# Performance work log

Hardware: AMD Instinct MI355X
Metric: run time of the kernel (lower is better)

Reference implementation:

```python
import jax, jax.numpy as jnp
import numpy as np

DIM = 768
HEADS = 12
HEAD_DIM = DIM // HEADS          # 64
DIM_HALF = HEAD_DIM // 2         # 32
SPATIAL = 3


def _rope_cos_sin(grid, voxel_size, theta):
    """grid: static tuple of ints (len SPATIAL); voxel_size: [SPATIAL] float;
    theta: [H, DIM_HALF] per-head frequency spectrum.
    Returns cos, sin of shape [H, N, DIM_HALF] where N = prod(grid)."""
    axes = [jnp.arange(g, dtype=theta.dtype) for g in grid]
    mesh = jnp.meshgrid(*axes, indexing='ij')
    coords = jnp.stack([m.reshape(-1) for m in mesh], axis=-1) * voxel_size  # [N, S] physical coords
    axis_idx = np.arange(DIM_HALF) % len(grid)        # round-robin freq->axis assignment
    pos = coords[:, axis_idx]                          # [N, DIM_HALF]
    ang = pos[None, :, :] * theta[:, None, :]          # [H, N, DIM_HALF]
    return jnp.cos(ang), jnp.sin(ang)


def _rope_apply(t, cos, sin):
    # t: [B, H, N, D]; cos/sin: [H, N, DIM_HALF] broadcast over batch
    t1, t2 = jnp.split(t, 2, axis=-1)
    return jnp.concatenate([t1 * cos - t2 * sin, t1 * sin + t2 * cos], axis=-1)


def setup_inputs() -> dict:
    key = jax.random.key(0)
    k_x, k_qkv, k_proj, k_b = jax.random.split(key, 4)
    B, N = 2, 8 * 16 * 16
    x = jax.random.normal(k_x, (B, N, DIM), dtype=jnp.float32)
    voxel_size = jnp.ones((SPATIAL,), dtype=jnp.float32)
    # nn.Linear weights are [out_features, in_features]
    w_qkv = jax.random.normal(k_qkv, (3 * DIM, DIM), dtype=jnp.float32) * (DIM ** -0.5)
    w_proj = jax.random.normal(k_proj, (DIM, DIM), dtype=jnp.float32) * (DIM ** -0.5)
    b_proj = jax.random.normal(k_b, (DIM,), dtype=jnp.float32) * 0.02
    # learnable per-head base frequencies: theta_j = 10000^{-j/dim_half}
    base = (1.0 / (10000.0 ** (np.arange(DIM_HALF, dtype=np.float32) / DIM_HALF)))
    theta = jnp.asarray(np.tile(base[None, :], (HEADS, 1)))  # [H, DIM_HALF]
    return {"x": x, "voxel_size": voxel_size, "w_qkv": w_qkv, "w_proj": w_proj,
            "b_proj": b_proj, "theta": theta, "grid_d": 8, "grid_h": 16, "grid_w": 16}


def reference(x, voxel_size, w_qkv, w_proj, b_proj, theta, grid_d, grid_h, grid_w):
    B, N, dim = x.shape
    H, D = HEADS, HEAD_DIM
    qkv = jnp.einsum('bnd,ed->bne', x, w_qkv).reshape(B, N, 3, H, D)
    qkv = jnp.transpose(qkv, (2, 0, 3, 1, 4))           # [3, B, H, N, D]
    q, k, v = qkv[0], qkv[1], qkv[2]
    cos, sin = _rope_cos_sin((grid_d, grid_h, grid_w), voxel_size, theta)
    q = _rope_apply(q, cos, sin)
    k = _rope_apply(k, cos, sin)
    scale = 1.0 / np.sqrt(D).astype(np.float32)
    attn = jax.nn.softmax(jnp.einsum('bhnd,bhmd->bhnm', q, k) * scale, axis=-1)
    out = jnp.einsum('bhnm,bhmd->bhnd', attn, v)        # [B, H, N, D]
    out = jnp.transpose(out, (0, 2, 1, 3)).reshape(B, N, dim)
    return out @ w_proj.T + b_proj
```

## Files before the change

kernel.cpp:

```cpp
#include <hip/hip_runtime.h>
#include <stdint.h>

#define DIM 768
#define NHEADS 12
#define HDIM 64
#define DHALF 32
#define NTOK 2048
#define QKVN 2304
#define LOG2E 1.44269504088896340736f

typedef unsigned short u16;
typedef unsigned int u32;
typedef __bf16 bf16x8 __attribute__((ext_vector_type(8)));
typedef short s16x8 __attribute__((ext_vector_type(8)));
typedef float f32x4 __attribute__((ext_vector_type(4)));

__device__ __forceinline__ f32x4 f4zero() { f32x4 z = {0.f, 0.f, 0.f, 0.f}; return z; }

__device__ __forceinline__ u16 f2bf(float f) {
    u32 u = __builtin_bit_cast(u32, f);
    u32 r = (u + 0x7FFFu + ((u >> 16) & 1u)) >> 16;
    return (u16)r;
}

__device__ __forceinline__ void gld_lds16(void* lds, const void* g) {
    __builtin_amdgcn_global_load_lds((const __attribute__((address_space(1))) u32*)g,
                                     (__attribute__((address_space(3))) u32*)lds,
                                     16, 0, 0);
}

__global__ __launch_bounds__(256) void cast3_f32_to_bf16(const float* __restrict__ a, u16* __restrict__ oa, int na4,
                                                         const float* __restrict__ b, u16* __restrict__ ob, int nb4,
                                                         const float* __restrict__ c, u16* __restrict__ oc, int nc4) {
    int i = blockIdx.x * 256 + threadIdx.x;
    const float* src;
    u16* dst;
    int j = i;
    if (i < na4) { src = a; dst = oa; }
    else if (i < na4 + nb4) { src = b; dst = ob; j = i - na4; }
    else if (i < na4 + nb4 + nc4) { src = c; dst = oc; j = i - na4 - nb4; }
    else return;
    float4 v = ((const float4*)src)[j];
    u32 w0 = (u32)f2bf(v.x) | ((u32)f2bf(v.y) << 16);
    u32 w1 = (u32)f2bf(v.z) | ((u32)f2bf(v.w) << 16);
    ((uint2*)dst)[j] = make_uint2(w0, w1);
}

__global__ __launch_bounds__(256) void gemm_bt(const u16* __restrict__ A, const u16* __restrict__ Bm,
                                               float* __restrict__ C, const float* __restrict__ bias,
                                               int M, int N, int K) {
    __shared__ __align__(16) u16 sA[2][128 * 32];
    __shared__ __align__(16) u16 sB[2][128 * 32];
    const int t = threadIdx.x;
    const int wave = t >> 6, lane = t & 63;
    const int quad = lane >> 4, l16 = lane & 15;
    const int bm = blockIdx.y * 128, bn = blockIdx.x * 128;
    const int wr = wave >> 1, wc = wave & 1;

    f32x4 acc[4][4];
#pragma unroll
    for (int i = 0; i < 4; i++)
#pragma unroll
        for (int j = 0; j < 4; j++) acc[i][j] = f4zero();

    auto stage = [&](int k0, int bi) {
#pragma unroll
        for (int r = 0; r < 2; ++r) {
            int c = (r * 4 + wave) * 64 + lane;
            int row = c >> 2, kc = c & 3;
            gld_lds16((char*)&sA[bi][0] + (size_t)(r * 4 + wave) * 1024,
                      A + (size_t)(bm + row) * K + k0 + kc * 8);
            gld_lds16((char*)&sB[bi][0] + (size_t)(r * 4 + wave) * 1024,
                      Bm + (size_t)(bn + row) * K + k0 + kc * 8);
        }
    };

    stage(0, 0);
    int cur = 0;
    for (int k0 = 0; k0 < K; k0 += 32) {
        __syncthreads();
        if (k0 + 32 < K) stage(k0 + 32, cur ^ 1);
        const u16* pA = &sA[cur][0];
        const u16* pB = &sB[cur][0];
        bf16x8 af[4], bfr[4];
#pragma unroll
        for (int mb = 0; mb < 4; mb++)
            af[mb] = *(const bf16x8*)(pA + (wr * 64 + mb * 16 + l16) * 32 + quad * 8);
#pragma unroll
        for (int nb = 0; nb < 4; nb++)
            bfr[nb] = *(const bf16x8*)(pB + (wc * 64 + nb * 16 + l16) * 32 + quad * 8);
#pragma unroll
        for (int mb = 0; mb < 4; mb++)
#pragma unroll
            for (int nb = 0; nb < 4; nb++)
                acc[mb][nb] = __builtin_amdgcn_mfma_f32_16x16x32_bf16(af[mb], bfr[nb], acc[mb][nb], 0, 0, 0);
        cur ^= 1;
    }
#pragma unroll
    for (int mb = 0; mb < 4; mb++)
#pragma unroll
        for (int nb = 0; nb < 4; nb++) {
            int col = bn + wc * 64 + nb * 16 + l16;
            float bv = bias ? bias[col] : 0.f;
#pragma unroll
            for (int r = 0; r < 4; r++) {
                int row = bm + wr * 64 + mb * 16 + quad * 4 + r;
                C[(size_t)row * N + col] = acc[mb][nb][r] + bv;
            }
        }
}

__global__ __launch_bounds__(256) void gemm_qkv_rope(const u16* __restrict__ A, const u16* __restrict__ Bm,
                                                     const float* __restrict__ voxel,
                                                     const float* __restrict__ theta,
                                                     const int* __restrict__ gh_p, const int* __restrict__ gw_p,
                                                     u16* __restrict__ q_s, u16* __restrict__ k_s,
                                                     u16* __restrict__ vT, int M) {
    __shared__ __align__(16) u16 sA[2][128 * 32];
    __shared__ __align__(16) u16 sB[2][128 * 32];
    const int t = threadIdx.x;
    const int wave = t >> 6, lane = t & 63;
    const int quad = lane >> 4, l16 = lane & 15;
    const int bm = blockIdx.y * 128, bn = blockIdx.x * 128;
    const int wr = wave >> 1, wc = wave & 1;
    const int K = DIM;

    f32x4 acc[4][4];
#pragma unroll
    for (int i = 0; i < 4; i++)
#pragma unroll
        for (int j = 0; j < 4; j++) acc[i][j] = f4zero();

    auto stage = [&](int k0, int bi) {
#pragma unroll
        for (int r = 0; r < 2; ++r) {
            int c = (r * 4 + wave) * 64 + lane;
            int row = c >> 2, kc = c & 3;
            gld_lds16((char*)&sA[bi][0] + (size_t)(r * 4 + wave) * 1024,
                      A + (size_t)(bm + row) * K + k0 + kc * 8);
            gld_lds16((char*)&sB[bi][0] + (size_t)(r * 4 + wave) * 1024,
                      Bm + (size_t)(bn + row) * K + k0 + kc * 8);
        }
    };

    stage(0, 0);
    int cur = 0;
    for (int k0 = 0; k0 < K; k0 += 32) {
        __syncthreads();
        if (k0 + 32 < K) stage(k0 + 32, cur ^ 1);
        const u16* pA = &sA[cur][0];
        const u16* pB = &sB[cur][0];
        bf16x8 af[4], bfr[4];
#pragma unroll
        for (int mb = 0; mb < 4; mb++)
            af[mb] = *(const bf16x8*)(pA + (wr * 64 + mb * 16 + l16) * 32 + quad * 8);
#pragma unroll
        for (int nb = 0; nb < 4; nb++)
            bfr[nb] = *(const bf16x8*)(pB + (wc * 64 + nb * 16 + l16) * 32 + quad * 8);
#pragma unroll
        for (int mb = 0; mb < 4; mb++)
#pragma unroll
            for (int nb = 0; nb < 4; nb++)
                acc[mb][nb] = __builtin_amdgcn_mfma_f32_16x16x32_bf16(af[mb], bfr[nb], acc[mb][nb], 0, 0, 0);
        cur ^= 1;
    }

    const int col0 = bn + wc * 64;
    const int typ = col0 / DIM;
    const int h = (col0 % DIM) >> 6;
    const int b = bm / NTOK;
    const int n0 = (bm % NTOK) + wr * 64;
    const size_t bh = (size_t)b * NHEADS + h;

    if (typ == 2) {
        int nt = n0 >> 6;
        u16* base = vT + (bh * 64 + (size_t)nt * 2) * 2048;
#pragma unroll
        for (int c2 = 0; c2 < 2; c2++)
#pragma unroll
            for (int nb = 0; nb < 4; nb++) {
                u32 w0 = (u32)f2bf(acc[2 * c2][nb][0]) | ((u32)f2bf(acc[2 * c2][nb][1]) << 16);
                u32 w1 = (u32)f2bf(acc[2 * c2][nb][2]) | ((u32)f2bf(acc[2 * c2][nb][3]) << 16);
                u32 w2 = (u32)f2bf(acc[2 * c2 + 1][nb][0]) | ((u32)f2bf(acc[2 * c2 + 1][nb][1]) << 16);
                u32 w3 = (u32)f2bf(acc[2 * c2 + 1][nb][2]) | ((u32)f2bf(acc[2 * c2 + 1][nb][3]) << 16);
                *(uint4*)(base + (size_t)c2 * 2048 + nb * 512 + lane * 8) = make_uint4(w0, w1, w2, w3);
            }
    } else {
        const int gh = *gh_p, gw = *gw_p;
        const float qsc = (typ == 0) ? 0.125f * LOG2E : 1.0f;
        const float th0 = theta[h * DHALF + l16];
        const float th1 = theta[h * DHALF + 16 + l16];
        const int ax0 = l16 % 3, ax1 = (16 + l16) % 3;
        const float vx0 = voxel[ax0], vx1 = voxel[ax1];
#pragma unroll
        for (int mb = 0; mb < 4; mb++)
#pragma unroll
            for (int r = 0; r < 4; r++) {
                int n = n0 + mb * 16 + quad * 4 + r;
                int xw = n % gw;
                int rem = n / gw;
                int yh = rem % gh;
                int zd = rem / gh;
                float c0 = (float)(ax0 == 0 ? zd : (ax0 == 1 ? yh : xw)) * vx0;
                float c1 = (float)(ax1 == 0 ? zd : (ax1 == 1 ? yh : xw)) * vx1;
                float s0, co0, s1, co1;
                __sincosf(c0 * th0, &s0, &co0);
                __sincosf(c1 * th1, &s1, &co1);
                float t1a = acc[mb][0][r], t2a = acc[mb][2][r];
                float o1a = (t1a * co0 - t2a * s0) * qsc, o2a = (t1a * s0 + t2a * co0) * qsc;
                float t1b = acc[mb][1][r], t2b = acc[mb][3][r];
                float o1b = (t1b * co1 - t2b * s1) * qsc, o2b = (t1b * s1 + t2b * co1) * qsc;
                if (typ == 0) {
                    u16* dq = q_s + (bh * NTOK + n) * HDIM;
                    dq[l16] = f2bf(o1a);
                    dq[l16 + DHALF] = f2bf(o2a);
                    dq[16 + l16] = f2bf(o1b);
                    dq[48 + l16] = f2bf(o2b);
                } else {
                    int tile_i = n >> 6;
                    int k16 = quad * 4 + r;
                    size_t baseo = bh * (size_t)NTOK * HDIM + (size_t)tile_i * 4096 + mb * 1024;
                    int j = l16 & 7;
                    size_t oa = baseo + (size_t)(((l16 >> 3) * 16 + k16) * 8 + j);
                    size_t ob = baseo + (size_t)((((2 + (l16 >> 3)) * 16) + k16) * 8 + j);
                    k_s[oa] = f2bf(o1a);
                    k_s[oa + 512] = f2bf(o2a);
                    k_s[ob] = f2bf(o1b);
                    k_s[ob + 512] = f2bf(o2b);
                }
            }
    }
}

__global__ __launch_bounds__(256) void flash_attn(const u16* __restrict__ Q, const u16* __restrict__ Kp,
                                                  const u16* __restrict__ Vp, u16* __restrict__ Out, int NBH) {
    int i = blockIdx.x;
    int bh_i = i % NBH;
    int qt = i / NBH;
    int b = bh_i / NHEADS, h = bh_i % NHEADS;
    int t = threadIdx.x, wave = t >> 6, lane = t & 63, quad = lane >> 4, l16 = lane & 15;
    size_t bh = (size_t)b * NHEADS + h;
    const u16* Qb = Q + bh * NTOK * HDIM;
    const u16* Kb = Kp + bh * NTOK * HDIM;
    const u16* Vb = Vp + bh * NTOK * HDIM;

    __shared__ __align__(16) u16 smem[2][8192];

    const int q0 = qt * 64 + wave * 16;
    bf16x8 qf[2];
#pragma unroll
    for (int kc = 0; kc < 2; kc++)
        qf[kc] = *(const bf16x8*)(Qb + (size_t)(q0 + l16) * HDIM + kc * 32 + quad * 8);

    s16x8 ov;
#pragma unroll
    for (int j = 0; j < 8; j++) ov[j] = (l16 == 0) ? (short)0x3F80 : (short)0;

    f32x4 o[5];
#pragma unroll
    for (int db = 0; db < 5; db++) o[db] = f4zero();

    auto stage = [&](int kt, int bi) {
        const u16* Kg = Kb + (size_t)kt * 4096;
        const u16* Vg = Vb + (size_t)kt * 4096;
        u16* buf = &smem[bi][0];
#pragma unroll
        for (int s = 0; s < 2; s++) {
            gld_lds16(buf + (wave * 2 + s) * 512, Kg + (wave * 2 + s) * 512 + lane * 8);
            gld_lds16(buf + 4096 + (wave * 2 + s) * 512, Vg + (wave * 2 + s) * 512 + lane * 8);
        }
    };

    stage(0, 0);
    int cur = 0;
    for (int kt = 0; kt < NTOK / 64; ++kt) {
        __syncthreads();
        if (kt + 1 < NTOK / 64) stage(kt + 1, cur ^ 1);
        const u16* sK = &smem[cur][0];
        const u16* sV = &smem[cur][4096];
#pragma unroll
        for (int c = 0; c < 2; ++c) {
            bf16x8 kf[2][2];
#pragma unroll
            for (int kb2 = 0; kb2 < 2; kb2++)
#pragma unroll
                for (int kc = 0; kc < 2; kc++)
                    kf[kb2][kc] = *(const bf16x8*)(sK + ((c * 2 + kb2) * 2 + kc) * 512 + lane * 8);
            s16x8 bv[4];
#pragma unroll
            for (int db = 0; db < 4; db++)
                bv[db] = *(const s16x8*)(sV + c * 2048 + db * 512 + lane * 8);
            f32x4 st0, st1;
            {
                f32x4 z = f4zero();
                z = __builtin_amdgcn_mfma_f32_16x16x32_bf16(kf[0][0], qf[0], z, 0, 0, 0);
                st0 = __builtin_amdgcn_mfma_f32_16x16x32_bf16(kf[0][1], qf[1], z, 0, 0, 0);
                f32x4 z2 = f4zero();
                z2 = __builtin_amdgcn_mfma_f32_16x16x32_bf16(kf[1][0], qf[0], z2, 0, 0, 0);
                st1 = __builtin_amdgcn_mfma_f32_16x16x32_bf16(kf[1][1], qf[1], z2, 0, 0, 0);
            }
            bf16x8 pb;
#pragma unroll
            for (int r = 0; r < 4; r++) {
                pb[r] = (__bf16)__builtin_exp2f(st0[r]);
                pb[r + 4] = (__bf16)__builtin_exp2f(st1[r]);
            }
#pragma unroll
            for (int db = 0; db < 4; db++)
                o[db] = __builtin_amdgcn_mfma_f32_16x16x32_bf16(pb, __builtin_bit_cast(bf16x8, bv[db]),
                                                                o[db], 0, 0, 0);
            o[4] = __builtin_amdgcn_mfma_f32_16x16x32_bf16(pb, __builtin_bit_cast(bf16x8, ov),
                                                           o[4], 0, 0, 0);
        }
        cur ^= 1;
    }

#pragma unroll
    for (int r = 0; r < 4; r++) {
        float s = __shfl(o[4][r], lane & 48);
        float inv = 1.0f / s;
        int n = q0 + quad * 4 + r;
        u16* dst = Out + ((size_t)b * NTOK + n) * DIM + h * HDIM + l16;
#pragma unroll
        for (int db = 0; db < 4; db++)
            dst[db * 16] = f2bf(o[db][r] * inv);
    }
}

extern "C" void kernel_launch(void* const* d_in, const int* in_sizes, int n_in,
                              void* d_out, int out_size, void* d_ws, size_t ws_size,
                              hipStream_t stream) {
    const float* x = (const float*)d_in[0];
    const float* voxel = (const float*)d_in[1];
    const float* w_qkv = (const float*)d_in[2];
    const float* w_proj = (const float*)d_in[3];
    const float* b_proj = (const float*)d_in[4];
    const float* theta = (const float*)d_in[5];
    const int* gh_p = (const int*)d_in[7];
    const int* gw_p = (const int*)d_in[8];
    const int B = in_sizes[0] / (NTOK * DIM);
    const int M = B * NTOK;

    char* p = (char*)d_ws;
    u16* xb = (u16*)p;       p += (size_t)M * DIM * 2;
    u16* wqkvb = (u16*)p;    p += (size_t)3 * DIM * DIM * 2;
    u16* wprojb = (u16*)p;   p += (size_t)DIM * DIM * 2;
    u16* q_s = (u16*)p;      p += (size_t)M * DIM * 2;
    u16* k_s = (u16*)p;      p += (size_t)M * DIM * 2;
    u16* vT = (u16*)p;       p += (size_t)M * DIM * 2;
    u16* attn = (u16*)p;     p += (size_t)M * DIM * 2;

    int na4 = M * DIM / 4, nb4 = 3 * DIM * DIM / 4, nc4 = DIM * DIM / 4;
    cast3_f32_to_bf16<<<dim3((na4 + nb4 + nc4 + 255) / 256), 256, 0, stream>>>(
        x, xb, na4, w_qkv, wqkvb, nb4, w_proj, wprojb, nc4);

    gemm_qkv_rope<<<dim3(QKVN / 128, M / 128), 256, 0, stream>>>(
        xb, wqkvb, voxel, theta, gh_p, gw_p, q_s, k_s, vT, M);

    flash_attn<<<dim3((B * NHEADS * NTOK) / 64), 256, 0, stream>>>(q_s, k_s, vT, attn, B * NHEADS);

    gemm_bt<<<dim3(DIM / 128, M / 128), 256, 0, stream>>>(attn, wprojb, (float*)d_out, b_proj, M, DIM, DIM);
}
```

Measured before the change: 180.4 us.

## Shrink GEMM tiles to raise block count for QKV and projection GEMMs

The output-projection GEMM moves from 128x128 tiles to 64x64 tiles, and the QKV+RoPE GEMM moves to 128x64 tiles with each wave owning 32 rows of a single head. The epilogue index math for the V-transpose and K-swizzle layouts is reworked to match the new wave ownership. The aim is to launch more blocks so the many compute units are better filled (the projection previously had only 192 blocks). The cost is less operand reuse per block and more global and LDS traffic per FLOP.

Measured after the change: 176.6 us. 1.02x faster.

```diff
diff --git a/kernel.cpp b/kernel.cpp
--- a/kernel.cpp
+++ b/kernel.cpp
@@ -49,30 +49,25 @@
 __global__ __launch_bounds__(256) void gemm_bt(const u16* __restrict__ A, const u16* __restrict__ Bm,
                                                float* __restrict__ C, const float* __restrict__ bias,
                                                int M, int N, int K) {
-    __shared__ __align__(16) u16 sA[2][128 * 32];
-    __shared__ __align__(16) u16 sB[2][128 * 32];
+    __shared__ __align__(16) u16 sA[2][64 * 32];
+    __shared__ __align__(16) u16 sB[2][64 * 32];
     const int t = threadIdx.x;
     const int wave = t >> 6, lane = t & 63;
     const int quad = lane >> 4, l16 = lane & 15;
-    const int bm = blockIdx.y * 128, bn = blockIdx.x * 128;
+    const int bm = blockIdx.y * 64, bn = blockIdx.x * 64;
     const int wr = wave >> 1, wc = wave & 1;
 
-    f32x4 acc[4][4];
-#pragma unroll
-    for (int i = 0; i < 4; i++)
-#pragma unroll
-        for (int j = 0; j < 4; j++) acc[i][j] = f4zero();
+    f32x4 acc[2][2];
+#pragma unroll
+    for (int i = 0; i < 2; i++)
+#pragma unroll
+        for (int j = 0; j < 2; j++) acc[i][j] = f4zero();
 
     auto stage = [&](int k0, int bi) {
-#pragma unroll
-        for (int r = 0; r < 2; ++r) {
-            int c = (r * 4 + wave) * 64 + lane;
-            int row = c >> 2, kc = c & 3;
-            gld_lds16((char*)&sA[bi][0] + (size_t)(r * 4 + wave) * 1024,
-                      A + (size_t)(bm + row) * K + k0 + kc * 8);
-            gld_lds16((char*)&sB[bi][0] + (size_t)(r * 4 + wave) * 1024,
-                      Bm + (size_t)(bn + row) * K + k0 + kc * 8);
-        }
+        gld_lds16((char*)&sA[bi][0] + wave * 1024,
+                  A + (size_t)(bm + wave * 16 + (lane >> 2)) * K + k0 + (lane & 3) * 8);
+        gld_lds16((char*)&sB[bi][0] + wave * 1024,
+                  Bm + (size_t)(bn + wave * 16 + (lane >> 2)) * K + k0 + (lane & 3) * 8);
     };
 
     stage(0, 0);
@@ -82,29 +77,29 @@
         if (k0 + 32 < K) stage(k0 + 32, cur ^ 1);
         const u16* pA = &sA[cur][0];
         const u16* pB = &sB[cur][0];
-        bf16x8 af[4], bfr[4];
-#pragma unroll
-        for (int mb = 0; mb < 4; mb++)
-            af[mb] = *(const bf16x8*)(pA + (wr * 64 + mb * 16 + l16) * 32 + quad * 8);
-#pragma unroll
-        for (int nb = 0; nb < 4; nb++)
-            bfr[nb] = *(const bf16x8*)(pB + (wc * 64 + nb * 16 + l16) * 32 + quad * 8);
-#pragma unroll
-        for (int mb = 0; mb < 4; mb++)
-#pragma unroll
-            for (int nb = 0; nb < 4; nb++)
+        bf16x8 af[2], bfr[2];
+#pragma unroll
+        for (int mb = 0; mb < 2; mb++)
+            af[mb] = *(const bf16x8*)(pA + (wr * 32 + mb * 16 + l16) * 32 + quad * 8);
+#pragma unroll
+        for (int nb = 0; nb < 2; nb++)
+            bfr[nb] = *(const bf16x8*)(pB + (wc * 32 + nb * 16 + l16) * 32 + quad * 8);
+#pragma unroll
+        for (int mb = 0; mb < 2; mb++)
+#pragma unroll
+            for (int nb = 0; nb < 2; nb++)
                 acc[mb][nb] = __builtin_amdgcn_mfma_f32_16x16x32_bf16(af[mb], bfr[nb], acc[mb][nb], 0, 0, 0);
         cur ^= 1;
     }
 #pragma unroll
-    for (int mb = 0; mb < 4; mb++)
-#pragma unroll
-        for (int nb = 0; nb < 4; nb++) {
-            int col = bn + wc * 64 + nb * 16 + l16;
+    for (int mb = 0; mb < 2; mb++)
+#pragma unroll
+        for (int nb = 0; nb < 2; nb++) {
+            int col = bn + wc * 32 + nb * 16 + l16;
             float bv = bias ? bias[col] : 0.f;
 #pragma unroll
             for (int r = 0; r < 4; r++) {
-                int row = bm + wr * 64 + mb * 16 + quad * 4 + r;
+                int row = bm + wr * 32 + mb * 16 + quad * 4 + r;
                 C[(size_t)row * N + col] = acc[mb][nb][r] + bv;
             }
         }
@@ -117,30 +112,28 @@
                                                      u16* __restrict__ q_s, u16* __restrict__ k_s,
                                                      u16* __restrict__ vT, int M) {
     __shared__ __align__(16) u16 sA[2][128 * 32];
-    __shared__ __align__(16) u16 sB[2][128 * 32];
+    __shared__ __align__(16) u16 sB[2][64 * 32];
     const int t = threadIdx.x;
     const int wave = t >> 6, lane = t & 63;
     const int quad = lane >> 4, l16 = lane & 15;
-    const int bm = blockIdx.y * 128, bn = blockIdx.x * 128;
-    const int wr = wave >> 1, wc = wave & 1;
+    const int bm = blockIdx.y * 128, bn = blockIdx.x * 64;
     const int K = DIM;
 
-    f32x4 acc[4][4];
-#pragma unroll
-    for (int i = 0; i < 4; i++)
+    f32x4 acc[2][4];
+#pragma unroll
+    for (int i = 0; i < 2; i++)
 #pragma unroll
         for (int j = 0; j < 4; j++) acc[i][j] = f4zero();
 
     auto stage = [&](int k0, int bi) {
 #pragma unroll
-        for (int r = 0; r < 2; ++r) {
-            int c = (r * 4 + wave) * 64 + lane;
-            int row = c >> 2, kc = c & 3;
-            gld_lds16((char*)&sA[bi][0] + (size_t)(r * 4 + wave) * 1024,
-                      A + (size_t)(bm + row) * K + k0 + kc * 8);
-            gld_lds16((char*)&sB[bi][0] + (size_t)(r * 4 + wave) * 1024,
-                      Bm + (size_t)(bn + row) * K + k0 + kc * 8);
-        }
+        for (int s = 0; s < 2; ++s) {
+            int ci = wave * 2 + s;
+            gld_lds16((char*)&sA[bi][0] + ci * 1024,
+                      A + (size_t)(bm + ci * 16 + (lane >> 2)) * K + k0 + (lane & 3) * 8);
+        }
+        gld_lds16((char*)&sB[bi][0] + wave * 1024,
+                  Bm + (size_t)(bn + wave * 16 + (lane >> 2)) * K + k0 + (lane & 3) * 8);
     };
 
     stage(0, 0);
@@ -150,41 +143,39 @@
         if (k0 + 32 < K) stage(k0 + 32, cur ^ 1);
         const u16* pA = &sA[cur][0];
         const u16* pB = &sB[cur][0];
-        bf16x8 af[4], bfr[4];
-#pragma unroll
-        for (int mb = 0; mb < 4; mb++)
-            af[mb] = *(const bf16x8*)(pA + (wr * 64 + mb * 16 + l16) * 32 + quad * 8);
+        bf16x8 af[2], bfr[4];
+#pragma unroll
+        for (int mb = 0; mb < 2; mb++)
+            af[mb] = *(const bf16x8*)(pA + (wave * 32 + mb * 16 + l16) * 32 + quad * 8);
 #pragma unroll
         for (int nb = 0; nb < 4; nb++)
-            bfr[nb] = *(const bf16x8*)(pB + (wc * 64 + nb * 16 + l16) * 32 + quad * 8);
-#pragma unroll
-        for (int mb = 0; mb < 4; mb++)
+            bfr[nb] = *(const bf16x8*)(pB + (nb * 16 + l16) * 32 + quad * 8);
+#pragma unroll
+        for (int mb = 0; mb < 2; mb++)
 #pragma unroll
             for (int nb = 0; nb < 4; nb++)
                 acc[mb][nb] = __builtin_amdgcn_mfma_f32_16x16x32_bf16(af[mb], bfr[nb], acc[mb][nb], 0, 0, 0);
         cur ^= 1;
     }
 
-    const int col0 = bn + wc * 64;
+    const int col0 = bn;
     const int typ = col0 / DIM;
     const int h = (col0 % DIM) >> 6;
     const int b = bm / NTOK;
-    const int n0 = (bm % NTOK) + wr * 64;
+    const int n0 = (bm % NTOK) + wave * 32;
     const size_t bh = (size_t)b * NHEADS + h;
 
     if (typ == 2) {
-        int nt = n0 >> 6;
-        u16* base = vT + (bh * 64 + (size_t)nt * 2) * 2048;
-#pragma unroll
-        for (int c2 = 0; c2 < 2; c2++)
-#pragma unroll
-            for (int nb = 0; nb < 4; nb++) {
-                u32 w0 = (u32)f2bf(acc[2 * c2][nb][0]) | ((u32)f2bf(acc[2 * c2][nb][1]) << 16);
-                u32 w1 = (u32)f2bf(acc[2 * c2][nb][2]) | ((u32)f2bf(acc[2 * c2][nb][3]) << 16);
-                u32 w2 = (u32)f2bf(acc[2 * c2 + 1][nb][0]) | ((u32)f2bf(acc[2 * c2 + 1][nb][1]) << 16);
-                u32 w3 = (u32)f2bf(acc[2 * c2 + 1][nb][2]) | ((u32)f2bf(acc[2 * c2 + 1][nb][3]) << 16);
-                *(uint4*)(base + (size_t)c2 * 2048 + nb * 512 + lane * 8) = make_uint4(w0, w1, w2, w3);
-            }
+        int chunk = ((bm % NTOK) >> 5) + wave;
+        u16* base = vT + ((size_t)bh * 64 + chunk) * 2048;
+#pragma unroll
+        for (int nb = 0; nb < 4; nb++) {
+            u32 w0 = (u32)f2bf(acc[0][nb][0]) | ((u32)f2bf(acc[0][nb][1]) << 16);
+            u32 w1 = (u32)f2bf(acc[0][nb][2]) | ((u32)f2bf(acc[0][nb][3]) << 16);
+            u32 w2 = (u32)f2bf(acc[1][nb][0]) | ((u32)f2bf(acc[1][nb][1]) << 16);
+            u32 w3 = (u32)f2bf(acc[1][nb][2]) | ((u32)f2bf(acc[1][nb][3]) << 16);
+            *(uint4*)(base + nb * 512 + lane * 8) = make_uint4(w0, w1, w2, w3);
+        }
     } else {
         const int gh = *gh_p, gw = *gw_p;
         const float qsc = (typ == 0) ? 0.125f * LOG2E : 1.0f;
@@ -193,7 +184,7 @@
         const int ax0 = l16 % 3, ax1 = (16 + l16) % 3;
         const float vx0 = voxel[ax0], vx1 = voxel[ax1];
 #pragma unroll
-        for (int mb = 0; mb < 4; mb++)
+        for (int mb = 0; mb < 2; mb++)
 #pragma unroll
             for (int r = 0; r < 4; r++) {
                 int n = n0 + mb * 16 + quad * 4 + r;
@@ -217,9 +208,11 @@
                     dq[16 + l16] = f2bf(o1b);
                     dq[48 + l16] = f2bf(o2b);
                 } else {
-                    int tile_i = n >> 6;
+                    int gm = wave * 2 + mb;
+                    int tile_i = ((bm % NTOK) >> 6) + (gm >> 2);
+                    int g = gm & 3;
                     int k16 = quad * 4 + r;
-                    size_t baseo = bh * (size_t)NTOK * HDIM + (size_t)tile_i * 4096 + mb * 1024;
+                    size_t baseo = bh * (size_t)NTOK * HDIM + (size_t)tile_i * 4096 + g * 1024;
                     int j = l16 & 7;
                     size_t oa = baseo + (size_t)(((l16 >> 3) * 16 + k16) * 8 + j);
                     size_t ob = baseo + (size_t)((((2 + (l16 >> 3)) * 16) + k16) * 8 + j);
@@ -354,10 +347,10 @@
     cast3_f32_to_bf16<<<dim3((na4 + nb4 + nc4 + 255) / 256), 256, 0, stream>>>(
         x, xb, na4, w_qkv, wqkvb, nb4, w_proj, wprojb, nc4);
 
-    gemm_qkv_rope<<<dim3(QKVN / 128, M / 128), 256, 0, stream>>>(
+    gemm_qkv_rope<<<dim3(QKVN / 64, M / 128), 256, 0, stream>>>(
         xb, wqkvb, voxel, theta, gh_p, gw_p, q_s, k_s, vT, M);
 
     flash_attn<<<dim3((B * NHEADS * NTOK) / 64), 256, 0, stream>>>(q_s, k_s, vT, attn, B * NHEADS);
 
-    gemm_bt<<<dim3(DIM / 128, M / 128), 256, 0, stream>>>(attn, wprojb, (float*)d_out, b_proj, M, DIM, DIM);
-}
+    gemm_bt<<<dim3(DIM / 64, M / 64), 256, 0, stream>>>(attn, wprojb, (float*)d_out, b_proj, M, DIM, DIM);
+}
```
